# Optimization experiments

Hardware: AMD Instinct MI355X
Metric: run time of the kernel (lower is better)

Reference implementation:

```python
import jax, jax.numpy as jnp
import numpy as np

B, N, D, H = 2, 2048, 1024, 16
DK = D // H
SCALE = DK ** -0.5


def setup_inputs() -> dict:
    key = jax.random.key(0)
    ks = jax.random.split(key, 11)
    s = D ** -0.5
    return {
        "q": jax.random.normal(ks[0], (B, N, D), jnp.float32),
        "k": jax.random.normal(ks[1], (B, N, D), jnp.float32),
        "v": jax.random.normal(ks[2], (B, N, D), jnp.float32),
        "Wq": jax.random.normal(ks[3], (D, D), jnp.float32) * s,
        "bq": jnp.zeros((D,), jnp.float32),
        "Wk": jax.random.normal(ks[4], (D, D), jnp.float32) * s,
        "bk": jnp.zeros((D,), jnp.float32),
        "Wv": jax.random.normal(ks[5], (D, D), jnp.float32) * s,
        "bv": jnp.zeros((D,), jnp.float32),
        "Wo": jax.random.normal(ks[6], (D, D), jnp.float32) * s,
        "bo": jnp.zeros((D,), jnp.float32),
    }


def _split_heads(x):
    # [b, n, h*d] -> [b, h, n, d]
    b, n, _ = x.shape
    return x.reshape(b, n, H, DK).transpose(0, 2, 1, 3)


def reference(q, k, v, Wq, bq, Wk, bk, Wv, bv, Wo, bo):
    qh = _split_heads(q @ Wq.T + bq)
    kh = _split_heads(k @ Wk.T + bk)
    vh = _split_heads(v @ Wv.T + bv)
    dots = jnp.einsum('bhid,bhjd->bhij', qh, kh) * SCALE
    attn = jax.nn.softmax(dots, axis=-1)
    out = jnp.einsum('bhij,bhjd->bhid', attn, vh)
    out = out.transpose(0, 2, 1, 3).reshape(q.shape[0], q.shape[1], D)
    return out @ Wo.T + bo
```

## Files before the change

kernel.cpp:

```cpp
#include <hip/hip_runtime.h>
#include <hip/hip_bf16.h>
#include <cstdint>
#include <cstddef>

#define BB 2
#define NN 2048
#define DD 1024
#define HH 16
#define DKK 64
#define SCALE 0.125f
#define LOG2E 1.4426950408889634f

typedef __bf16 bf16;
typedef __bf16 bf16x4 __attribute__((ext_vector_type(4)));
typedef __bf16 bf16x8 __attribute__((ext_vector_type(8)));
typedef float f32x4 __attribute__((ext_vector_type(4)));
typedef short s16x4 __attribute__((ext_vector_type(4)));

#define GLD(gp, lp)                                                            \
  __builtin_amdgcn_global_load_lds(                                            \
      (const __attribute__((address_space(1))) void*)(gp),                     \
      (__attribute__((address_space(3))) void*)(lp), 16, 0, 0)

struct CvtArgs { const float* s[7]; bf16* d[7]; int n[7]; };

__global__ void k_cvt(CvtArgs a) {
  const int seg = blockIdx.y;
  const float* __restrict__ s = a.s[seg];
  bf16* __restrict__ d = a.d[seg];
  int i = (blockIdx.x * 256 + threadIdx.x) * 8;
  if (i >= a.n[seg]) return;
  float4 f0 = *(const float4*)(s + i);
  float4 f1 = *(const float4*)(s + i + 4);
  bf16x8 o;
  o[0] = (bf16)f0.x; o[1] = (bf16)f0.y; o[2] = (bf16)f0.z; o[3] = (bf16)f0.w;
  o[4] = (bf16)f1.x; o[5] = (bf16)f1.y; o[6] = (bf16)f1.z; o[7] = (bf16)f1.w;
  *(bf16x8*)(d + i) = o;
}

template <int BN>
__device__ __forceinline__ void gemm_body(
    const bf16* __restrict__ A, const bf16* __restrict__ W,
    const float* __restrict__ bias, bf16* __restrict__ outB,
    float* __restrict__ outF, int mode, float oscale, int m0, int n0) {
  const int K = 1024;
  constexpr int NI = BN / 32;
  constexpr int BI = BN * 8 / 256;
  __shared__ bf16 lA[128 * 64];
  __shared__ bf16 lB[BN * 64];
  const int t = threadIdx.x;
  const int lane = t & 63, quad = lane >> 4, l16 = lane & 15, w = t >> 6;
  const int wm = (w >> 1) * 64, wn = (w & 1) * (BN / 2);

  f32x4 acc[4][NI] = {};

  const bf16* gA[4]; const bf16* gB[BI];
#pragma unroll
  for (int i4 = 0; i4 < 4; i4++) {
    int i = i4 * 256 + t;
    int r = i >> 3, c = (i & 7) ^ (r & 7);
    gA[i4] = A + (size_t)(m0 + r) * K + c * 8;
  }
#pragma unroll
  for (int i4 = 0; i4 < BI; i4++) {
    int i = i4 * 256 + t;
    int r = i >> 3, c = (i & 7) ^ (r & 7);
    gB[i4] = W + (size_t)(n0 + r) * K + c * 8;
  }

  for (int kb = 0; kb < K; kb += 64) {
    __syncthreads();
#pragma unroll
    for (int i4 = 0; i4 < 4; i4++) GLD(gA[i4] + kb, lA + (i4 * 256 + t) * 8);
#pragma unroll
    for (int i4 = 0; i4 < BI; i4++) GLD(gB[i4] + kb, lB + (i4 * 256 + t) * 8);
    __syncthreads();

#pragma unroll
    for (int kb2 = 0; kb2 < 2; kb2++) {
      bf16x8 af[4], bfr[NI];
      const int ch = ((kb2 * 4 + quad) ^ (l16 & 7)) * 8;
#pragma unroll
      for (int i = 0; i < 4; i++)
        af[i] = *(const bf16x8*)(lA + (wm + i * 16 + l16) * 64 + ch);
#pragma unroll
      for (int i = 0; i < NI; i++)
        bfr[i] = *(const bf16x8*)(lB + (wn + i * 16 + l16) * 64 + ch);
#pragma unroll
      for (int mi = 0; mi < 4; mi++)
#pragma unroll
        for (int ni = 0; ni < NI; ni++)
          acc[mi][ni] = __builtin_amdgcn_mfma_f32_16x16x32_bf16(
              af[mi], bfr[ni], acc[mi][ni], 0, 0, 0);
    }
  }

#pragma unroll
  for (int mi = 0; mi < 4; mi++) {
#pragma unroll
    for (int ni = 0; ni < NI; ni++) {
#pragma unroll
      for (int r = 0; r < 4; r++) {
        int gm = m0 + wm + mi * 16 + quad * 4 + r;
        int gn = n0 + wn + ni * 16 + l16;
        float v = (acc[mi][ni][r] + bias[gn]) * oscale;
        if (mode == 3) {
          outF[(size_t)gm * 1024 + gn] = v;
        } else {
          int b = gm >> 11, row = gm & 2047;
          int h = gn >> 6, dk = gn & 63;
          if (mode == 2)
            outB[((size_t)(b * HH + h) * DKK + dk) * NN + row] = (bf16)v;
          else
            outB[((size_t)(b * HH + h) * NN + row) * DKK + dk] = (bf16)v;
        }
      }
    }
  }
}

struct QkvArgs {
  const bf16* A; const bf16* W; const float* b[3]; bf16* o[3]; float sc0;
};

__global__ __launch_bounds__(256, 3) void k_qkv(QkvArgs g) {
  const int z = blockIdx.z;
  gemm_body<128>(g.A + (size_t)z * 4194304, g.W + (size_t)z * 1048576,
                 g.b[z], g.o[z], nullptr, z == 2 ? 2 : 0,
                 z == 0 ? g.sc0 : 1.0f, blockIdx.x * 128, blockIdx.y * 128);
}

__global__ __launch_bounds__(256, 4) void k_oproj(
    const bf16* __restrict__ A, const bf16* __restrict__ W,
    const float* __restrict__ bias, float* __restrict__ out) {
  gemm_body<64>(A, W, bias, nullptr, out, 3, 1.0f, blockIdx.x * 128,
                blockIdx.y * 64);
}

__global__ __launch_bounds__(512, 4) void k_attn(
    const bf16* __restrict__ Qp, const bf16* __restrict__ Kp,
    const bf16* __restrict__ Vt, bf16* __restrict__ Ao) {
  __shared__ bf16 lK[2][128 * 64];
  __shared__ bf16 lV[2][64 * 128];
  const int t = threadIdx.x;
  const int lane = t & 63, quad = lane >> 4, l16 = lane & 15, w = t >> 6;
  const int wq = w & 3;
  const int kh = w >> 2;
  const int bh = blockIdx.x;
  const int qt = blockIdx.y;
  const bf16* Qb = Qp + (size_t)bh * NN * DKK;
  const bf16* Kb = Kp + (size_t)bh * NN * DKK;
  const bf16* Vb = Vt + (size_t)bh * DKK * NN;

  const int qr0 = qt * 128 + wq * 32;
  bf16x8 qf[2][2];
#pragma unroll
  for (int j = 0; j < 2; j++)
#pragma unroll
    for (int kq = 0; kq < 2; kq++)
      qf[j][kq] = *(const bf16x8*)(Qb + (size_t)(qr0 + j * 16 + l16) * DKK +
                                   kq * 32 + quad * 8);

  float lj[2] = {0.f, 0.f};
  f32x4 oaccT[2][4] = {};

  const bf16* gK[2]; const bf16* gV[2];
#pragma unroll
  for (int i2 = 0; i2 < 2; i2++) {
    int i = i2 * 512 + t;
    int rK = i >> 3, cK = (i & 7) ^ (rK & 7);
    gK[i2] = Kb + (size_t)rK * DKK + cK * 8;
    int rV = i >> 4, cV = (i & 15) ^ (rV & 15);
    gV[i2] = Vb + (size_t)rV * NN + cV * 8;
  }
  const int swzK0 = (quad ^ (l16 & 7)) * 8;
  const int swzK1 = ((4 + quad) ^ (l16 & 7)) * 8;

#pragma unroll
  for (int i2 = 0; i2 < 2; i2++) {
    GLD(gK[i2], &lK[0][(i2 * 512 + t) * 8]);
    GLD(gV[i2], &lV[0][(i2 * 512 + t) * 8]);
  }

  int p = 0;
  for (int kt = 0; kt < NN; kt += 128) {
    __syncthreads();
    if (kt + 128 < NN) {
#pragma unroll
      for (int i2 = 0; i2 < 2; i2++) {
        GLD(gK[i2] + (size_t)(kt + 128) * DKK, &lK[p ^ 1][(i2 * 512 + t) * 8]);
        GLD(gV[i2] + (kt + 128), &lV[p ^ 1][(i2 * 512 + t) * 8]);
      }
    }

    f32x4 s[2][4];
#pragma unroll
    for (int tt = 0; tt < 4; tt++) {
      const bf16* kbase = &lK[p][((kh * 4 + tt) * 16 + l16) * 64];
      bf16x8 kf0 = *(const bf16x8*)(kbase + swzK0);
      bf16x8 kf1 = *(const bf16x8*)(kbase + swzK1);
#pragma unroll
      for (int j = 0; j < 2; j++) {
        f32x4 z = {0.f, 0.f, 0.f, 0.f};
        z = __builtin_amdgcn_mfma_f32_16x16x32_bf16(kf0, qf[j][0], z, 0, 0, 0);
        z = __builtin_amdgcn_mfma_f32_16x16x32_bf16(kf1, qf[j][1], z, 0, 0, 0);
        s[j][tt] = z;
      }
    }

    s16x4 pa[2][4];
#pragma unroll
    for (int j = 0; j < 2; j++) {
      float rs = 0.f;
#pragma unroll
      for (int tt = 0; tt < 4; tt++) {
        bf16x4 pb;
#pragma unroll
        for (int r = 0; r < 4; r++) {
          float pe = __builtin_amdgcn_exp2f(s[j][tt][r]);
          rs += pe;
          pb[r] = (bf16)pe;
        }
        pa[j][tt] = __builtin_bit_cast(s16x4, pb);
      }
      lj[j] += rs;
    }

#pragma unroll
    for (int tt = 0; tt < 4; tt++) {
#pragma unroll
      for (int ni = 0; ni < 4; ni++) {
        int rv = ni * 16 + l16;
        int cc = kh * 8 + 2 * tt + (quad >> 1);
        const bf16* vaddr =
            &lV[p][rv * 128 + ((cc ^ l16) * 8) + (quad & 1) * 4];
        s16x4 vb = __builtin_bit_cast(s16x4, *(const bf16x4*)vaddr);
#pragma unroll
        for (int j = 0; j < 2; j++)
          oaccT[j][ni] = __builtin_amdgcn_mfma_f32_16x16x16bf16_1k(
              vb, pa[j][tt], oaccT[j][ni], 0, 0, 0);
      }
    }
    p ^= 1;
  }

  __syncthreads();
  float* redO = (float*)&lK[0][0];
  float* redL = (float*)&lV[0][0];
  if (kh == 1) {
    float* dst = redO + (wq * 64 + lane) * 32;
#pragma unroll
    for (int j = 0; j < 2; j++)
#pragma unroll
      for (int ni = 0; ni < 4; ni++)
        *(f32x4*)(dst + (j * 4 + ni) * 4) = oaccT[j][ni];
    redL[(wq * 64 + lane) * 2 + 0] = lj[0];
    redL[(wq * 64 + lane) * 2 + 1] = lj[1];
  }
  __syncthreads();
  if (kh == 0) {
    const float* src = redO + (wq * 64 + lane) * 32;
#pragma unroll
    for (int j = 0; j < 2; j++)
#pragma unroll
      for (int ni = 0; ni < 4; ni++)
        oaccT[j][ni] += *(const f32x4*)(src + (j * 4 + ni) * 4);
    lj[0] += redL[(wq * 64 + lane) * 2 + 0];
    lj[1] += redL[(wq * 64 + lane) * 2 + 1];

    const int b = bh >> 4, h = bh & 15;
#pragma unroll
    for (int j = 0; j < 2; j++) {
      float l = lj[j];
      l += __shfl_xor(l, 16);
      l += __shfl_xor(l, 32);
      const float inv = 1.0f / l;
      bf16* dst = Ao + ((size_t)(b * NN) + qr0 + j * 16 + l16) * DD +
                  h * DKK + quad * 4;
#pragma unroll
      for (int ni = 0; ni < 4; ni++) {
        bf16x4 ov;
#pragma unroll
        for (int r = 0; r < 4; r++) ov[r] = (bf16)(oaccT[j][ni][r] * inv);
        *(bf16x4*)(dst + ni * 16) = ov;
      }
    }
  }
}

extern "C" void kernel_launch(void* const* d_in, const int* in_sizes, int n_in,
                              void* d_out, int out_size, void* d_ws,
                              size_t ws_size, hipStream_t stream) {
  const float* qin = (const float*)d_in[0];
  const float* kin = (const float*)d_in[1];
  const float* vin = (const float*)d_in[2];
  const float* Wq = (const float*)d_in[3];
  const float* bq = (const float*)d_in[4];
  const float* Wk = (const float*)d_in[5];
  const float* bk = (const float*)d_in[6];
  const float* Wv = (const float*)d_in[7];
  const float* bv = (const float*)d_in[8];
  const float* Wo = (const float*)d_in[9];
  const float* bo = (const float*)d_in[10];
  float* out = (float*)d_out;

  const int MN = BB * NN * DD;
  const int WNel = DD * DD;
  bf16* ws = (bf16*)d_ws;
  bf16* Xb = ws;
  bf16* Wb = Xb + 3 * MN;
  bf16* Qp = Wb + 4 * WNel;
  bf16* Kp = Qp + MN;
  bf16* Vt = Kp + MN;
  bf16* Ao = Xb;

  CvtArgs ca{{qin, kin, vin, Wq, Wk, Wv, Wo},
             {Xb, Xb + MN, Xb + 2 * MN, Wb, Wb + WNel, Wb + 2 * WNel,
              Wb + 3 * WNel},
             {MN, MN, MN, WNel, WNel, WNel, WNel}};
  k_cvt<<<dim3(2048, 7), 256, 0, stream>>>(ca);

  QkvArgs g{Xb, Wb, {bq, bk, bv}, {Qp, Kp, Vt}, SCALE * LOG2E};
  k_qkv<<<dim3(32, 8, 3), 256, 0, stream>>>(g);
  k_attn<<<dim3(32, 16), 512, 0, stream>>>(Qp, Kp, Vt, Ao);
  k_oproj<<<dim3(32, 16), 256, 0, stream>>>(Ao, Wb + 3 * WNel, bo, out);
}
```

Measured before the change: 223.6 us.

## Stage transposed V projection output through LDS and raise priority around MFMA blocks

```diff
diff --git a/kernel.cpp b/kernel.cpp
--- a/kernel.cpp
+++ b/kernel.cpp
@@ -95,6 +95,40 @@
     }
   }
 
+  if (mode == 2) {
+    __syncthreads();
+    bf16* scr = (w < 2 ? lA : lB) + (w & 1) * 4096;
+#pragma unroll
+    for (int ni = 0; ni < NI; ni++) {
+      int c = ni * 16 + l16;
+      float bs = bias[n0 + wn + c];
+#pragma unroll
+      for (int mi = 0; mi < 4; mi++) {
+        int u = (mi * 2 + (quad >> 1)) ^ (c & 7);
+        bf16x4 pv;
+#pragma unroll
+        for (int r = 0; r < 4; r++)
+          pv[r] = (bf16)((acc[mi][ni][r] + bs) * oscale);
+        *(bf16x4*)(scr + c * 64 + u * 8 + (quad & 1) * 4) = pv;
+      }
+    }
+    __syncthreads();
+    {
+      const int gm0 = m0 + wm;
+      const int b = gm0 >> 11, row0 = gm0 & 2047;
+#pragma unroll
+      for (int it = 0; it < 8; it++) {
+        int c = it * 8 + (lane >> 3);
+        int u = (lane & 7) ^ (lane >> 3);
+        bf16x8 val = *(const bf16x8*)(scr + c * 64 + u * 8);
+        int gn = n0 + wn + c;
+        int h = gn >> 6, dk = gn & 63;
+        *(bf16x8*)(outB + ((size_t)(b * HH + h) * DKK + dk) * NN + row0 +
+                   (lane & 7) * 8) = val;
+      }
+    }
+    return;
+  }
 #pragma unroll
   for (int mi = 0; mi < 4; mi++) {
 #pragma unroll
@@ -109,10 +143,7 @@
         } else {
           int b = gm >> 11, row = gm & 2047;
           int h = gn >> 6, dk = gn & 63;
-          if (mode == 2)
-            outB[((size_t)(b * HH + h) * DKK + dk) * NN + row] = (bf16)v;
-          else
-            outB[((size_t)(b * HH + h) * NN + row) * DKK + dk] = (bf16)v;
+          outB[((size_t)(b * HH + h) * NN + row) * DKK + dk] = (bf16)v;
         }
       }
     }
@@ -194,6 +225,7 @@
     }
 
     f32x4 s[2][4];
+    __builtin_amdgcn_s_setprio(1);
 #pragma unroll
     for (int tt = 0; tt < 4; tt++) {
       const bf16* kbase = &lK[p][((kh * 4 + tt) * 16 + l16) * 64];
@@ -207,6 +239,7 @@
         s[j][tt] = z;
       }
     }
+    __builtin_amdgcn_s_setprio(0);
 
     s16x4 pa[2][4];
 #pragma unroll
@@ -226,6 +259,7 @@
       lj[j] += rs;
     }
 
+    __builtin_amdgcn_s_setprio(1);
 #pragma unroll
     for (int tt = 0; tt < 4; tt++) {
 #pragma unroll
@@ -241,6 +275,7 @@
               vb, pa[j][tt], oaccT[j][ni], 0, 0, 0);
       }
     }
+    __builtin_amdgcn_s_setprio(0);
     p ^= 1;
   }
 
```

Result: faster. 213.9 us (-4.4%).
